# Performance work log

Hardware: AMD Instinct MI355X
Metric: run time of the kernel (lower is better)

The kernel has to match this reference:

```python
import jax, jax.numpy as jnp
from jax import lax
import numpy as np

B, P, T = 2048, 128, 64     # batch, program len, trace len
V, NC, NO = 1000, 32, 16    # token vocab, n choice names, options per choice
E, H = 300, 256             # embedding size, hidden size
GIN = H + 2 * E             # GRUCell input size = 856


def setup_inputs() -> dict:
    key = jax.random.key(0)
    ks = jax.random.split(key, 20)
    g = lambda k, shape, fan: jax.random.normal(k, shape, jnp.float32) / np.sqrt(fan)
    return {
        "program": jax.random.randint(ks[0], (B, P), 0, V),
        "program_len": jax.random.randint(ks[1], (B,), 1, P + 1),
        "trace": jax.random.randint(ks[2], (B, T), 0, NC),
        "trace_len": jax.random.randint(ks[3], (B,), 1, T + 1),
        "choices": jax.random.randint(ks[4], (B, NC), 0, NO),
        "h0_enc": jax.random.normal(ks[5], (B, H), jnp.float32) * 0.06,  # xavier-ish init of h0
        "h0_dec": jax.random.normal(ks[6], (B, H), jnp.float32) * 0.06,
        "token_emb": jax.random.normal(ks[7], (V, E), jnp.float32) * 0.02,
        "Wih_enc": g(ks[8], (H, E), E),      # vanilla RNN (tanh)
        "Whh_enc": g(ks[9], (H, H), H),
        "bih_enc": jnp.zeros((H,), jnp.float32),
        "bhh_enc": jnp.zeros((H,), jnp.float32),
        "choice_tab": jax.random.normal(ks[10], (NC, NO, E), jnp.float32) * 0.02,
        "index_tab": jax.random.normal(ks[11], (NC, E), jnp.float32) * 0.02,
        "Wih_gru": g(ks[12], (3 * H, GIN), GIN),
        "Whh_gru": g(ks[13], (3 * H, H), H),
        "bih_gru": jnp.zeros((3 * H,), jnp.float32),
        "bhh_gru": jnp.zeros((3 * H,), jnp.float32),
        "infW": g(ks[14], (NC, NO, H), H),   # per-choice-name Linear(H -> NO)
        "infb": jnp.zeros((NC, NO), jnp.float32),
    }


def _encode(program, program_len, h0, token_emb, Wih, Whh, bih, bhh):
    # ProgramEncoder: embedding -> packed tanh-RNN -> final hidden per sequence
    xs = jnp.swapaxes(token_emb[program], 0, 1)            # [P, B, E] time-major
    mask = jnp.arange(P)[:, None] < program_len[None, :]   # [P, B] valid steps

    def step(h, inp):
        x_t, m_t = inp
        h_new = jnp.tanh(x_t @ Wih.T + bih + h @ Whh.T + bhh)
        return jnp.where(m_t[:, None], h_new, h), None

    h_final, _ = lax.scan(step, h0, (xs, mask))
    return h_final  # [B, H]


def reference(program, program_len, trace, trace_len, choices, h0_enc, h0_dec,
              token_emb, Wih_enc, Whh_enc, bih_enc, bhh_enc,
              choice_tab, index_tab, Wih_gru, Whh_gru, bih_gru, bhh_gru,
              infW, infb):
    prog_h = _encode(program, program_len, h0_enc, token_emb,
                     Wih_enc, Whh_enc, bih_enc, bhh_enc)      # [B, H]

    prev_seq = jnp.swapaxes(trace[:, :-1], 0, 1)  # [T-1, B] choice-name at step i
    cur_seq = jnp.swapaxes(trace[:, 1:], 0, 1)    # [T-1, B] choice-name at step i+1
    barange = jnp.arange(B)

    def dec_step(h, inp):
        prev, cur = inp                           # [B] ints
        idx_e = index_tab[prev]                   # [B, E]
        opt = choices[barange, prev]              # gather(dim=1) of chosen option
        ch_e = choice_tab[prev, opt]              # [B, E]
        x = jnp.concatenate([ch_e, prog_h, idx_e], axis=-1)  # [B, GIN]
        # GRUCell (torch gate order r, z, n)
        gx = x @ Wih_gru.T + bih_gru              # [B, 3H]
        gh = h @ Whh_gru.T + bhh_gru
        xr, xz, xn = jnp.split(gx, 3, axis=-1)
        hr, hz, hn = jnp.split(gh, 3, axis=-1)
        r = jax.nn.sigmoid(xr + hr)
        z = jax.nn.sigmoid(xz + hz)
        n = jnp.tanh(xn + r * hn)
        h_new = (1.0 - z) * n + z * h
        # per-choice-name inference head selected by cur_choice
        pred = jnp.einsum('bh,boh->bo', h_new, infW[cur]) + infb[cur]  # [B, NO]
        return h_new, pred

    _, preds = lax.scan(dec_step, h0_dec, (prev_seq, cur_seq))
    return preds  # [T-1, B, NO]
```

## Files before the change

kernel.cpp:

```cpp
#include <hip/hip_runtime.h>


typedef unsigned short ushort_t;
typedef short short8 __attribute__((ext_vector_type(8)));
typedef float f32x4_t __attribute__((ext_vector_type(4)));

#define NB_ 128

__device__ __forceinline__ ushort_t f32_to_bf16_rne(float f){
    unsigned int u = __float_as_uint(f);
    unsigned int r = u + 0x7fffu + ((u >> 16) & 1u);
    return (ushort_t)(r >> 16);
}
__device__ __forceinline__ float b2f(ushort_t s){
    return __uint_as_float(((unsigned int)s) << 16);
}
__device__ __forceinline__ void split2(float x, ushort_t &hh, ushort_t &hl){
    hh = f32_to_bf16_rne(x);
    float r = x - b2f(hh);
    hl = f32_to_bf16_rne(r);
}
__device__ __forceinline__ f32x4_t mfma16(uint4 a, uint4 b, f32x4_t c){
    return __builtin_amdgcn_mfma_f32_16x16x32_bf16(
        __builtin_bit_cast(short8, a), __builtin_bit_cast(short8, b), c, 0, 0, 0);
}
__device__ __forceinline__ float sigm(float x){
    return __fdividef(1.f, 1.f + __expf(-x));
}
__device__ __forceinline__ float tanh_f(float x){
    return 1.f - __fdividef(2.f, 1.f + __expf(2.f * x));
}

__global__ void prep_kernel(
    const float* __restrict__ Whh_enc, const float* __restrict__ Whh_gru,
    const float* __restrict__ Wih_gru, const float* __restrict__ token_emb,
    const float* __restrict__ Wih_enc, const float* __restrict__ bih_enc,
    const float* __restrict__ bhh_enc, const float* __restrict__ index_tab,
    const float* __restrict__ bih_gru, const float* __restrict__ bhh_gru,
    const float* __restrict__ choice_tab,
    ushort_t* __restrict__ enc_h, ushort_t* __restrict__ enc_l,
    ushort_t* __restrict__ gru_h, ushort_t* __restrict__ gru_l,
    ushort_t* __restrict__ mid_h, ushort_t* __restrict__ mid_l,
    float* __restrict__ tok_proj, float* __restrict__ xproj)
{
    __shared__ __align__(16) float s_a[304];
    __shared__ __align__(16) float s_b[304];
    const int tid = threadIdx.x;
    const int bid = blockIdx.x;

    if (bid < 1792){
        const int idx = bid * 256 + tid;
        float v; ushort_t *ph, *pl; int fi;
        if (idx < 65536){
            fi = idx;
            const int m = fi & 7, lane = (fi >> 3) & 63, t2 = fi >> 9;
            const int nt = t2 & 15, kt = t2 >> 4;
            const int k = (kt << 5) + ((lane >> 4) << 3) + m;
            const int j = (nt << 4) + (lane & 15);
            v = Whh_enc[(j << 8) + k]; ph = enc_h; pl = enc_l;
        } else if (idx < 262144){
            fi = idx - 65536;
            const int m = fi & 7, lane = (fi >> 3) & 63, t2 = fi >> 9;
            const int nt = t2 % 48, kt = t2 / 48;
            const int k = (kt << 5) + ((lane >> 4) << 3) + m;
            const int j = (nt << 4) + (lane & 15);
            v = Whh_gru[(j << 8) + k]; ph = gru_h; pl = gru_l;
        } else {
            fi = idx - 262144;
            const int m = fi & 7, lane = (fi >> 3) & 63, t2 = fi >> 9;
            const int nt = t2 % 48, kt = t2 / 48;
            const int k = (kt << 5) + ((lane >> 4) << 3) + m;
            const int j = (nt << 4) + (lane & 15);
            v = Wih_gru[j * 856 + 300 + k]; ph = mid_h; pl = mid_l;
        }
        ushort_t hh, hl; split2(v, hh, hl);
        ph[fi] = hh; pl[fi] = hl;
    } else if (bid < 3328){
        const int b2 = bid - 1792;
        const int co = b2 / 3, part = b2 - co * 3;
        const int c = co >> 4;
        const int g = part * 256 + tid;
        for (int i2 = tid; i2 < 300; i2 += 256){
            s_a[i2] = choice_tab[co * 300 + i2];
            s_b[i2] = index_tab[c * 300 + i2];
        }
        __syncthreads();
        float acc = bih_gru[g] + (g < 512 ? bhh_gru[g] : 0.f);
        const f32x4_t* wa = (const f32x4_t*)(Wih_gru + g * 856);
        const f32x4_t* wb = (const f32x4_t*)(Wih_gru + g * 856 + 556);
        const f32x4_t* xa = (const f32x4_t*)s_a;
        const f32x4_t* xb = (const f32x4_t*)s_b;
        #pragma unroll 5
        for (int e = 0; e < 75; ++e){
            f32x4_t a = xa[e], w0 = wa[e], b = xb[e], w1 = wb[e];
            acc += a[0]*w0[0] + a[1]*w0[1] + a[2]*w0[2] + a[3]*w0[3]
                 + b[0]*w1[0] + b[1]*w1[1] + b[2]*w1[2] + b[3]*w1[3];
        }
        xproj[co * 768 + g] = acc;
    } else {
        const int v0 = bid - 3328;
        for (int i2 = tid; i2 < 300; i2 += 256) s_a[i2] = token_emb[v0 * 300 + i2];
        __syncthreads();
        float acc = bih_enc[tid] + bhh_enc[tid];
        const f32x4_t* wa = (const f32x4_t*)(Wih_enc + tid * 300);
        const f32x4_t* xa = (const f32x4_t*)s_a;
        #pragma unroll 5
        for (int e = 0; e < 75; ++e){
            f32x4_t a = xa[e], b = wa[e];
            acc += a[0]*b[0] + a[1]*b[1] + a[2]*b[2] + a[3]*b[3];
        }
        tok_proj[(v0 << 8) + tid] = acc;
    }
}

__global__ __launch_bounds__(256, 1) void enc_kernel(
    const int* __restrict__ program, const int* __restrict__ plen,
    const float* __restrict__ h0, const float* __restrict__ tokproj,
    const ushort_t* __restrict__ enc_h, const ushort_t* __restrict__ enc_l,
    const ushort_t* __restrict__ mid_h, const ushort_t* __restrict__ mid_l,
    float* __restrict__ prog_proj)
{
    __shared__ __align__(16) ushort_t hbuf[2][2][16 * 256];
    __shared__ int prog_s[16 * 128];
    const int tid = threadIdx.x, bid = blockIdx.x;
    const int wave = tid >> 6, lane = tid & 63;
    const int r0 = bid << 4;

    for (int i = tid; i < 2048; i += 256) prog_s[i] = program[(r0 << 7) + i];

    const int rowbase = (lane >> 4) << 2;
    const int jbase = (wave << 6) + (lane & 15);
    int plen_r[4];
    #pragma unroll
    for (int i = 0; i < 4; ++i) plen_r[i] = plen[r0 + rowbase + i];

    const uint4* __restrict__ be_h = (const uint4*)enc_h;
    const uint4* __restrict__ be_l = (const uint4*)enc_l;
    uint4 bh_r[8][4], bl_r[8][4];
    #pragma unroll
    for (int kt = 0; kt < 8; ++kt)
    #pragma unroll
    for (int q = 0; q < 4; ++q){
        const int fo = (((kt << 4) + (wave << 2) + q) << 6) + lane;
        bh_r[kt][q] = be_h[fo];
        bl_r[kt][q] = be_l[fo];
    }

    float hreg[4][4];
    #pragma unroll
    for (int q = 0; q < 4; ++q)
    #pragma unroll
    for (int i = 0; i < 4; ++i){
        const int row = rowbase + i, j = jbase + (q << 4);
        float v = h0[((r0 + row) << 8) + j];
        hreg[q][i] = v;
        ushort_t hh, hl; split2(v, hh, hl);
        const int b0 = (((row << 9) + (j << 1)) ^ ((row & 7) << 4)) >> 1;
        hbuf[0][0][b0] = hh; hbuf[0][1][b0] = hl;
    }
    __syncthreads();

    const int arow = lane & 15;
    const int abase = (arow << 9) + ((lane >> 4) << 4);
    const int asw = (arow & 7) << 4;
    int cur = 0;

    for (int t = 0; t < 128; ++t){
        f32x4_t acc[4];
        int tok[4];
        #pragma unroll
        for (int i = 0; i < 4; ++i) tok[i] = prog_s[((rowbase + i) << 7) + t];
        #pragma unroll
        for (int q = 0; q < 4; ++q)
        #pragma unroll
        for (int i = 0; i < 4; ++i)
            acc[q][i] = tokproj[(tok[i] << 8) + jbase + (q << 4)];

        #pragma unroll
        for (int kt = 0; kt < 8; ++kt){
            const int b = ((abase + (kt << 6)) ^ asw) >> 1;
            const uint4 ah = *(const uint4*)&hbuf[cur][0][b];
            const uint4 al = *(const uint4*)&hbuf[cur][1][b];
            #pragma unroll
            for (int q = 0; q < 4; ++q){
                f32x4_t c = acc[q];
                c = mfma16(ah, bh_r[kt][q], c);
                c = mfma16(al, bh_r[kt][q], c);
                c = mfma16(ah, bl_r[kt][q], c);
                acc[q] = c;
            }
        }
        const int nb = cur ^ 1;
        #pragma unroll
        for (int q = 0; q < 4; ++q)
        #pragma unroll
        for (int i = 0; i < 4; ++i){
            const int row = rowbase + i, j = jbase + (q << 4);
            float v = (t < plen_r[i]) ? tanh_f(acc[q][i]) : hreg[q][i];
            hreg[q][i] = v;
            ushort_t hh, hl; split2(v, hh, hl);
            const int b0 = (((row << 9) + (j << 1)) ^ ((row & 7) << 4)) >> 1;
            hbuf[nb][0][b0] = hh; hbuf[nb][1][b0] = hl;
        }
        cur = nb;
        __syncthreads();
    }

    uint4 ahr[8], alr[8];
    #pragma unroll
    for (int kt = 0; kt < 8; ++kt){
        const int b = ((abase + (kt << 6)) ^ asw) >> 1;
        ahr[kt] = *(const uint4*)&hbuf[cur][0][b];
        alr[kt] = *(const uint4*)&hbuf[cur][1][b];
    }
    const uint4* __restrict__ bm_h = (const uint4*)mid_h;
    const uint4* __restrict__ bm_l = (const uint4*)mid_l;
    f32x4_t pacc[12];
    #pragma unroll
    for (int u = 0; u < 12; ++u){ f32x4_t z = {0.f,0.f,0.f,0.f}; pacc[u] = z; }
    #pragma unroll
    for (int kt = 0; kt < 8; ++kt){
        #pragma unroll
        for (int u = 0; u < 12; ++u){
            const int nt = wave * 12 + u;
            const int fo = ((kt * 48 + nt) << 6) + lane;
            const uint4 bh = bm_h[fo], bl = bm_l[fo];
            f32x4_t c = pacc[u];
            c = mfma16(ahr[kt], bh, c);
            c = mfma16(alr[kt], bh, c);
            c = mfma16(ahr[kt], bl, c);
            pacc[u] = c;
        }
    }
    #pragma unroll
    for (int u = 0; u < 12; ++u){
        const int g = (wave * 12 + u) * 16 + (lane & 15);
        #pragma unroll
        for (int i = 0; i < 4; ++i)
            prog_proj[(r0 + rowbase + i) * 768 + g] = pacc[u][i];
    }
}

__global__ __launch_bounds__(256, 1) void dec_kernel(
    const int* __restrict__ trace, const int* __restrict__ choices,
    const float* __restrict__ h0, const float* __restrict__ prog_proj,
    const float* __restrict__ xproj,
    const ushort_t* __restrict__ gru_h, const ushort_t* __restrict__ gru_l,
    const float* __restrict__ bhh_gru, const float* __restrict__ infW,
    const float* __restrict__ infb, float* __restrict__ out)
{
    __shared__ __align__(16) ushort_t hbuf[2][2][16 * 256];
    __shared__ __align__(16) float pred_lds[16 * 272];
    __shared__ int trace_s[16 * 64];
    __shared__ int choice_s[16 * 32];
    const int tid = threadIdx.x, bid = blockIdx.x;
    const int wave = tid >> 6, lane = tid & 63;
    const int r0 = bid << 4;

    for (int i = tid; i < 1024; i += 256) trace_s[i] = trace[(r0 << 6) + i];
    for (int i = tid; i < 512; i += 256) choice_s[i] = choices[(r0 << 5) + i];

    const int rowbase = (lane >> 4) << 2;
    const int jbase = (wave << 6) + (lane & 15);

    float hreg[4][4];
    float bhhn[4];
    #pragma unroll
    for (int q = 0; q < 4; ++q) bhhn[q] = bhh_gru[512 + jbase + (q << 4)];

    float ppr[3][4][4];
    #pragma unroll
    for (int g3 = 0; g3 < 3; ++g3)
    #pragma unroll
    for (int q = 0; q < 4; ++q)
    #pragma unroll
    for (int i = 0; i < 4; ++i)
        ppr[g3][q][i] = prog_proj[(r0 + rowbase + i) * 768 + (g3 << 8) + jbase + (q << 4)];

    #pragma unroll
    for (int q = 0; q < 4; ++q)
    #pragma unroll
    for (int i = 0; i < 4; ++i){
        const int row = rowbase + i, j = jbase + (q << 4);
        float v = h0[((r0 + row) << 8) + j];
        hreg[q][i] = v;
        ushort_t hh, hl; split2(v, hh, hl);
        const int b0 = (((row << 9) + (j << 1)) ^ ((row & 7) << 4)) >> 1;
        hbuf[0][0][b0] = hh; hbuf[0][1][b0] = hl;
    }
    __syncthreads();

    const uint4* __restrict__ bg_h = (const uint4*)gru_h;
    const uint4* __restrict__ bg_l = (const uint4*)gru_l;
    const int arow = lane & 15;
    const int abase = (arow << 9) + ((lane >> 4) << 4);
    const int asw = (arow & 7) << 4;
    int cur = 0;

    for (int t = 0; t < 63; ++t){
        int prev_i[4], opt_i[4];
        #pragma unroll
        for (int i = 0; i < 4; ++i){
            const int row = rowbase + i;
            prev_i[i] = trace_s[(row << 6) + t];
            opt_i[i] = choice_s[(row << 5) + prev_i[i]];
        }
        f32x4_t acc[3][4];
        float xn[4][4];
        #pragma unroll
        for (int i = 0; i < 4; ++i){
            const float* xp = xproj + ((prev_i[i] << 4) + opt_i[i]) * 768;
            #pragma unroll
            for (int q = 0; q < 4; ++q){
                const int j = jbase + (q << 4);
                acc[0][q][i] = xp[j]       + ppr[0][q][i];
                acc[1][q][i] = xp[256 + j] + ppr[1][q][i];
                xn[q][i]     = xp[512 + j] + ppr[2][q][i];
                acc[2][q][i] = bhhn[q];
            }
        }
        uint4 ahr[8], alr[8];
        #pragma unroll
        for (int kt = 0; kt < 8; ++kt){
            const int b = ((abase + (kt << 6)) ^ asw) >> 1;
            ahr[kt] = *(const uint4*)&hbuf[cur][0][b];
            alr[kt] = *(const uint4*)&hbuf[cur][1][b];
        }
        #pragma unroll
        for (int kt = 0; kt < 8; ++kt){
            #pragma unroll
            for (int g3 = 0; g3 < 3; ++g3)
            #pragma unroll
            for (int q = 0; q < 4; ++q){
                const int nt = (g3 << 4) + (wave << 2) + q;
                const int fo = ((kt * 48 + nt) << 6) + lane;
                const uint4 bh = bg_h[fo], bl = bg_l[fo];
                f32x4_t c = acc[g3][q];
                c = mfma16(ahr[kt], bh, c);
                c = mfma16(alr[kt], bh, c);
                c = mfma16(ahr[kt], bl, c);
                acc[g3][q] = c;
            }
        }
        const int nb = cur ^ 1;
        #pragma unroll
        for (int q = 0; q < 4; ++q)
        #pragma unroll
        for (int i = 0; i < 4; ++i){
            const float r = sigm(acc[0][q][i]);
            const float z = sigm(acc[1][q][i]);
            const float n = tanh_f(xn[q][i] + r * acc[2][q][i]);
            const float hv = (1.f - z) * n + z * hreg[q][i];
            hreg[q][i] = hv;
            ushort_t hh, hl; split2(hv, hh, hl);
            const int row = rowbase + i, j = jbase + (q << 4);
            const int b0 = (((row << 9) + (j << 1)) ^ ((row & 7) << 4)) >> 1;
            hbuf[nb][0][b0] = hh; hbuf[nb][1][b0] = hl;
        }
        __syncthreads();

        {
            const int prow = tid >> 4, ks = tid & 15;
            const int ct = trace_s[(prow << 6) + t + 1];
            const int psw = (prow & 7) << 4;
            const int hb = (prow << 9) + (ks << 5);
            union { uint4 v; ushort_t s[8]; } H0, H1, L0, L1;
            H0.v = *(const uint4*)&hbuf[nb][0][((hb) ^ psw) >> 1];
            H1.v = *(const uint4*)&hbuf[nb][0][((hb + 16) ^ psw) >> 1];
            L0.v = *(const uint4*)&hbuf[nb][1][((hb) ^ psw) >> 1];
            L1.v = *(const uint4*)&hbuf[nb][1][((hb + 16) ^ psw) >> 1];
            float hv[16];
            #pragma unroll
            for (int n2 = 0; n2 < 8; ++n2){
                hv[n2]     = b2f(H0.s[n2]) + b2f(L0.s[n2]);
                hv[8 + n2] = b2f(H1.s[n2]) + b2f(L1.s[n2]);
            }
            const float* iwb = infW + ((size_t)ct << 12) + (ks << 4);
            #pragma unroll
            for (int o = 0; o < 16; ++o){
                const f32x4_t* wp = (const f32x4_t*)(iwb + (o << 8));
                const f32x4_t w0 = wp[0], w1 = wp[1], w2 = wp[2], w3 = wp[3];
                float s =
                    hv[0]*w0[0] + hv[1]*w0[1] + hv[2]*w0[2] + hv[3]*w0[3]
                  + hv[4]*w1[0] + hv[5]*w1[1] + hv[6]*w1[2] + hv[7]*w1[3]
                  + hv[8]*w2[0] + hv[9]*w2[1] + hv[10]*w2[2] + hv[11]*w2[3]
                  + hv[12]*w3[0]+ hv[13]*w3[1]+ hv[14]*w3[2]+ hv[15]*w3[3];
                pred_lds[prow * 272 + (o << 4) + ks] = s;
            }
        }
        __syncthreads();
        {
            const int rrow = tid >> 4, oo = tid & 15;
            float s = 0.f;
            #pragma unroll
            for (int k2 = 0; k2 < 16; ++k2) s += pred_lds[rrow * 272 + (oo << 4) + k2];
            const int ct2 = trace_s[(rrow << 6) + t + 1];
            s += infb[(ct2 << 4) + oo];
            out[(size_t)t * 32768 + ((size_t)(r0 + rrow) << 4) + oo] = s;
        }
        cur = nb;
    }
}

extern "C" void kernel_launch(void* const* d_in, const int* in_sizes, int n_in,
                              void* d_out, int out_size, void* d_ws, size_t ws_size,
                              hipStream_t stream)
{
    const int*   program   = (const int*)  d_in[0];
    const int*   plen      = (const int*)  d_in[1];
    const int*   trace     = (const int*)  d_in[2];
    const int*   choices   = (const int*)  d_in[4];
    const float* h0_enc    = (const float*)d_in[5];
    const float* h0_dec    = (const float*)d_in[6];
    const float* token_emb = (const float*)d_in[7];
    const float* Wih_enc   = (const float*)d_in[8];
    const float* Whh_enc   = (const float*)d_in[9];
    const float* bih_enc   = (const float*)d_in[10];
    const float* bhh_enc   = (const float*)d_in[11];
    const float* choice_tab= (const float*)d_in[12];
    const float* index_tab = (const float*)d_in[13];
    const float* Wih_gru   = (const float*)d_in[14];
    const float* Whh_gru   = (const float*)d_in[15];
    const float* bih_gru   = (const float*)d_in[16];
    const float* bhh_gru   = (const float*)d_in[17];
    const float* infW      = (const float*)d_in[18];
    const float* infb      = (const float*)d_in[19];
    float* out = (float*)d_out;

    char* w = (char*)d_ws;
    ushort_t* enc_h = (ushort_t*)(w + 0);
    ushort_t* enc_l = (ushort_t*)(w + 131072);
    ushort_t* gru_h = (ushort_t*)(w + 262144);
    ushort_t* gru_l = (ushort_t*)(w + 655360);
    ushort_t* mid_h = (ushort_t*)(w + 1048576);
    ushort_t* mid_l = (ushort_t*)(w + 1441792);
    float* tok_proj = (float*)(w + 1835008);
    float* xproj    = (float*)(w + 2859008);
    float* prog_proj= (float*)(w + 4431872);

    prep_kernel<<<4328, 256, 0, stream>>>(
        Whh_enc, Whh_gru, Wih_gru, token_emb, Wih_enc, bih_enc, bhh_enc,
        index_tab, bih_gru, bhh_gru, choice_tab,
        enc_h, enc_l, gru_h, gru_l, mid_h, mid_l,
        tok_proj, xproj);

    enc_kernel<<<NB_, 256, 0, stream>>>(
        program, plen, h0_enc, tok_proj, enc_h, enc_l, mid_h, mid_l, prog_proj);

    dec_kernel<<<NB_, 256, 0, stream>>>(
        trace, choices, h0_dec, prog_proj, xproj,
        gru_h, gru_l, bhh_gru, infW, infb, out);
}
```

Before: 3.648 ms.

## Retile GRU decoder to 32 rows per block and prefetch encoder token projections

```diff
diff --git a/kernel.cpp b/kernel.cpp
--- a/kernel.cpp
+++ b/kernel.cpp
@@ -4,8 +4,6 @@
 typedef unsigned short ushort_t;
 typedef short short8 __attribute__((ext_vector_type(8)));
 typedef float f32x4_t __attribute__((ext_vector_type(4)));
-
-#define NB_ 128
 
 __device__ __forceinline__ ushort_t f32_to_bf16_rne(float f){
     unsigned int u = __float_as_uint(f);
@@ -165,16 +163,36 @@
     const int asw = (arow & 7) << 4;
     int cur = 0;
 
+    float nxt[4][4];
+    {
+        int tok[4];
+        #pragma unroll
+        for (int i = 0; i < 4; ++i) tok[i] = prog_s[((rowbase + i) << 7)];
+        #pragma unroll
+        for (int q = 0; q < 4; ++q)
+        #pragma unroll
+        for (int i = 0; i < 4; ++i)
+            nxt[q][i] = tokproj[(tok[i] << 8) + jbase + (q << 4)];
+    }
+
     for (int t = 0; t < 128; ++t){
         f32x4_t acc[4];
-        int tok[4];
-        #pragma unroll
-        for (int i = 0; i < 4; ++i) tok[i] = prog_s[((rowbase + i) << 7) + t];
         #pragma unroll
         for (int q = 0; q < 4; ++q)
         #pragma unroll
         for (int i = 0; i < 4; ++i)
-            acc[q][i] = tokproj[(tok[i] << 8) + jbase + (q << 4)];
+            acc[q][i] = nxt[q][i];
+
+        if (t < 127){
+            int tok[4];
+            #pragma unroll
+            for (int i = 0; i < 4; ++i) tok[i] = prog_s[((rowbase + i) << 7) + t + 1];
+            #pragma unroll
+            for (int q = 0; q < 4; ++q)
+            #pragma unroll
+            for (int i = 0; i < 4; ++i)
+                nxt[q][i] = tokproj[(tok[i] << 8) + jbase + (q << 4)];
+        }
 
         #pragma unroll
         for (int kt = 0; kt < 8; ++kt){
@@ -241,7 +259,7 @@
     }
 }
 
-__global__ __launch_bounds__(256, 1) void dec_kernel(
+__global__ __launch_bounds__(512, 2) void dec_kernel(
     const int* __restrict__ trace, const int* __restrict__ choices,
     const float* __restrict__ h0, const float* __restrict__ prog_proj,
     const float* __restrict__ xproj,
@@ -249,45 +267,39 @@
     const float* __restrict__ bhh_gru, const float* __restrict__ infW,
     const float* __restrict__ infb, float* __restrict__ out)
 {
-    __shared__ __align__(16) ushort_t hbuf[2][2][16 * 256];
-    __shared__ __align__(16) float pred_lds[16 * 272];
-    __shared__ int trace_s[16 * 64];
-    __shared__ int choice_s[16 * 32];
+    __shared__ __align__(16) ushort_t hbuf[2][32 * 256];
+    __shared__ int trace_s[32 * 64];
+    __shared__ int choice_s[32 * 32];
     const int tid = threadIdx.x, bid = blockIdx.x;
     const int wave = tid >> 6, lane = tid & 63;
-    const int r0 = bid << 4;
-
-    for (int i = tid; i < 1024; i += 256) trace_s[i] = trace[(r0 << 6) + i];
-    for (int i = tid; i < 512; i += 256) choice_s[i] = choices[(r0 << 5) + i];
-
-    const int rowbase = (lane >> 4) << 2;
-    const int jbase = (wave << 6) + (lane & 15);
-
-    float hreg[4][4];
-    float bhhn[4];
-    #pragma unroll
-    for (int q = 0; q < 4; ++q) bhhn[q] = bhh_gru[512 + jbase + (q << 4)];
-
-    float ppr[3][4][4];
-    #pragma unroll
-    for (int g3 = 0; g3 < 3; ++g3)
-    #pragma unroll
-    for (int q = 0; q < 4; ++q)
-    #pragma unroll
-    for (int i = 0; i < 4; ++i)
-        ppr[g3][q][i] = prog_proj[(r0 + rowbase + i) * 768 + (g3 << 8) + jbase + (q << 4)];
-
-    #pragma unroll
-    for (int q = 0; q < 4; ++q)
-    #pragma unroll
-    for (int i = 0; i < 4; ++i){
-        const int row = rowbase + i, j = jbase + (q << 4);
+    const int r0 = bid << 5;
+
+    for (int i = tid; i < 2048; i += 512) trace_s[i] = trace[(r0 << 6) + i];
+    for (int i = tid; i < 1024; i += 512) choice_s[i] = choices[(r0 << 5) + i];
+
+    #pragma unroll
+    for (int e = 0; e < 16; ++e){
+        const int i = (e << 9) + tid;
+        const int row = i >> 8, j = i & 255;
         float v = h0[((r0 + row) << 8) + j];
-        hreg[q][i] = v;
         ushort_t hh, hl; split2(v, hh, hl);
         const int b0 = (((row << 9) + (j << 1)) ^ ((row & 7) << 4)) >> 1;
-        hbuf[0][0][b0] = hh; hbuf[0][1][b0] = hl;
-    }
+        hbuf[0][b0] = hh; hbuf[1][b0] = hl;
+    }
+
+    const int crow = (lane >> 4) << 2;
+    const int jcol = (wave << 5) + (lane & 15);
+    float bhhn[2];
+    #pragma unroll
+    for (int jt = 0; jt < 2; ++jt) bhhn[jt] = bhh_gru[512 + jcol + (jt << 4)];
+    float hreg[2][2][4];
+    #pragma unroll
+    for (int rt = 0; rt < 2; ++rt)
+    #pragma unroll
+    for (int jt = 0; jt < 2; ++jt)
+    #pragma unroll
+    for (int rg = 0; rg < 4; ++rg)
+        hreg[rt][jt][rg] = h0[((r0 + (rt << 4) + crow + rg) << 8) + jcol + (jt << 4)];
     __syncthreads();
 
     const uint4* __restrict__ bg_h = (const uint4*)gru_h;
@@ -295,67 +307,96 @@
     const int arow = lane & 15;
     const int abase = (arow << 9) + ((lane >> 4) << 4);
     const int asw = (arow & 7) << 4;
-    int cur = 0;
 
     for (int t = 0; t < 63; ++t){
-        int prev_i[4], opt_i[4];
-        #pragma unroll
-        for (int i = 0; i < 4; ++i){
-            const int row = rowbase + i;
-            prev_i[i] = trace_s[(row << 6) + t];
-            opt_i[i] = choice_s[(row << 5) + prev_i[i]];
-        }
-        f32x4_t acc[3][4];
-        float xn[4][4];
-        #pragma unroll
-        for (int i = 0; i < 4; ++i){
-            const float* xp = xproj + ((prev_i[i] << 4) + opt_i[i]) * 768;
-            #pragma unroll
-            for (int q = 0; q < 4; ++q){
-                const int j = jbase + (q << 4);
-                acc[0][q][i] = xp[j]       + ppr[0][q][i];
-                acc[1][q][i] = xp[256 + j] + ppr[1][q][i];
-                xn[q][i]     = xp[512 + j] + ppr[2][q][i];
-                acc[2][q][i] = bhhn[q];
-            }
-        }
-        uint4 ahr[8], alr[8];
-        #pragma unroll
-        for (int kt = 0; kt < 8; ++kt){
-            const int b = ((abase + (kt << 6)) ^ asw) >> 1;
-            ahr[kt] = *(const uint4*)&hbuf[cur][0][b];
-            alr[kt] = *(const uint4*)&hbuf[cur][1][b];
-        }
-        #pragma unroll
-        for (int kt = 0; kt < 8; ++kt){
-            #pragma unroll
-            for (int g3 = 0; g3 < 3; ++g3)
-            #pragma unroll
-            for (int q = 0; q < 4; ++q){
-                const int nt = (g3 << 4) + (wave << 2) + q;
-                const int fo = ((kt * 48 + nt) << 6) + lane;
-                const uint4 bh = bg_h[fo], bl = bg_l[fo];
-                f32x4_t c = acc[g3][q];
-                c = mfma16(ahr[kt], bh, c);
-                c = mfma16(alr[kt], bh, c);
-                c = mfma16(ahr[kt], bl, c);
-                acc[g3][q] = c;
-            }
-        }
-        const int nb = cur ^ 1;
-        #pragma unroll
-        for (int q = 0; q < 4; ++q)
-        #pragma unroll
-        for (int i = 0; i < 4; ++i){
-            const float r = sigm(acc[0][q][i]);
-            const float z = sigm(acc[1][q][i]);
-            const float n = tanh_f(xn[q][i] + r * acc[2][q][i]);
-            const float hv = (1.f - z) * n + z * hreg[q][i];
-            hreg[q][i] = hv;
-            ushort_t hh, hl; split2(hv, hh, hl);
-            const int row = rowbase + i, j = jbase + (q << 4);
+        f32x4_t acc[3][2][2];
+        #pragma unroll
+        for (int rt = 0; rt < 2; ++rt)
+        #pragma unroll
+        for (int jt = 0; jt < 2; ++jt){
+            f32x4_t z4 = {0.f, 0.f, 0.f, 0.f};
+            acc[0][rt][jt] = z4; acc[1][rt][jt] = z4;
+            f32x4_t bn = {bhhn[jt], bhhn[jt], bhhn[jt], bhhn[jt]};
+            acc[2][rt][jt] = bn;
+        }
+
+        float xv[3][2][2][4];
+        #pragma unroll
+        for (int half = 0; half < 2; ++half){
+            if (half == 1){
+                #pragma unroll
+                for (int rt = 0; rt < 2; ++rt)
+                #pragma unroll
+                for (int rg = 0; rg < 4; ++rg){
+                    const int lrow = (rt << 4) + crow + rg;
+                    const int prev = trace_s[(lrow << 6) + t];
+                    const int opt = choice_s[(lrow << 5) + prev];
+                    const float* xb = xproj + ((prev << 4) + opt) * 768;
+                    const float* pb = prog_proj + (r0 + lrow) * 768;
+                    #pragma unroll
+                    for (int g = 0; g < 3; ++g)
+                    #pragma unroll
+                    for (int jt = 0; jt < 2; ++jt){
+                        const int jj = (g << 8) + jcol + (jt << 4);
+                        xv[g][rt][jt][rg] = xb[jj] + pb[jj];
+                    }
+                }
+            }
+            #pragma unroll
+            for (int kt4 = 0; kt4 < 4; ++kt4){
+                const int kt = (half << 2) + kt4;
+                uint4 ah[2], al[2];
+                #pragma unroll
+                for (int rt = 0; rt < 2; ++rt){
+                    const int b = (((rt << 13) + abase + (kt << 6)) ^ asw) >> 1;
+                    ah[rt] = *(const uint4*)&hbuf[0][b];
+                    al[rt] = *(const uint4*)&hbuf[1][b];
+                }
+                #pragma unroll
+                for (int g = 0; g < 3; ++g)
+                #pragma unroll
+                for (int jt = 0; jt < 2; ++jt){
+                    const int nt = (g << 4) + (wave << 1) + jt;
+                    const int fo = ((kt * 48 + nt) << 6) + lane;
+                    const uint4 bh = bg_h[fo], bl = bg_l[fo];
+                    #pragma unroll
+                    for (int rt = 0; rt < 2; ++rt){
+                        f32x4_t c = acc[g][rt][jt];
+                        c = mfma16(ah[rt], bh, c);
+                        c = mfma16(al[rt], bh, c);
+                        c = mfma16(ah[rt], bl, c);
+                        acc[g][rt][jt] = c;
+                    }
+                }
+            }
+        }
+
+        ushort_t wh[2][2][4], wl[2][2][4];
+        #pragma unroll
+        for (int rt = 0; rt < 2; ++rt)
+        #pragma unroll
+        for (int jt = 0; jt < 2; ++jt)
+        #pragma unroll
+        for (int rg = 0; rg < 4; ++rg){
+            const float rr = sigm(acc[0][rt][jt][rg] + xv[0][rt][jt][rg]);
+            const float zz = sigm(acc[1][rt][jt][rg] + xv[1][rt][jt][rg]);
+            const float nn = tanh_f(xv[2][rt][jt][rg] + rr * acc[2][rt][jt][rg]);
+            const float hv = (1.f - zz) * nn + zz * hreg[rt][jt][rg];
+            hreg[rt][jt][rg] = hv;
+            split2(hv, wh[rt][jt][rg], wl[rt][jt][rg]);
+        }
+        __syncthreads();
+        #pragma unroll
+        for (int rt = 0; rt < 2; ++rt)
+        #pragma unroll
+        for (int jt = 0; jt < 2; ++jt)
+        #pragma unroll
+        for (int rg = 0; rg < 4; ++rg){
+            const int row = (rt << 4) + crow + rg;
+            const int j = jcol + (jt << 4);
             const int b0 = (((row << 9) + (j << 1)) ^ ((row & 7) << 4)) >> 1;
-            hbuf[nb][0][b0] = hh; hbuf[nb][1][b0] = hl;
+            hbuf[0][b0] = wh[rt][jt][rg];
+            hbuf[1][b0] = wl[rt][jt][rg];
         }
         __syncthreads();
 
@@ -363,42 +404,45 @@
             const int prow = tid >> 4, ks = tid & 15;
             const int ct = trace_s[(prow << 6) + t + 1];
             const int psw = (prow & 7) << 4;
-            const int hb = (prow << 9) + (ks << 5);
-            union { uint4 v; ushort_t s[8]; } H0, H1, L0, L1;
-            H0.v = *(const uint4*)&hbuf[nb][0][((hb) ^ psw) >> 1];
-            H1.v = *(const uint4*)&hbuf[nb][0][((hb + 16) ^ psw) >> 1];
-            L0.v = *(const uint4*)&hbuf[nb][1][((hb) ^ psw) >> 1];
-            L1.v = *(const uint4*)&hbuf[nb][1][((hb + 16) ^ psw) >> 1];
-            float hv[16];
+            const int ba = (((prow << 9) + (ks << 5)) ^ psw) >> 1;
+            const int bb = (((prow << 9) + (ks << 5) + 16) ^ psw) >> 1;
+            union { uint4 v; ushort_t u[8]; } H0, H1, L0, L1;
+            H0.v = *(const uint4*)&hbuf[0][ba];
+            H1.v = *(const uint4*)&hbuf[0][bb];
+            L0.v = *(const uint4*)&hbuf[1][ba];
+            L1.v = *(const uint4*)&hbuf[1][bb];
+            float hv16[16];
             #pragma unroll
             for (int n2 = 0; n2 < 8; ++n2){
-                hv[n2]     = b2f(H0.s[n2]) + b2f(L0.s[n2]);
-                hv[8 + n2] = b2f(H1.s[n2]) + b2f(L1.s[n2]);
+                hv16[n2]     = b2f(H0.u[n2]) + b2f(L0.u[n2]);
+                hv16[8 + n2] = b2f(H1.u[n2]) + b2f(L1.u[n2]);
             }
             const float* iwb = infW + ((size_t)ct << 12) + (ks << 4);
+            float s[16];
             #pragma unroll
             for (int o = 0; o < 16; ++o){
                 const f32x4_t* wp = (const f32x4_t*)(iwb + (o << 8));
                 const f32x4_t w0 = wp[0], w1 = wp[1], w2 = wp[2], w3 = wp[3];
-                float s =
-                    hv[0]*w0[0] + hv[1]*w0[1] + hv[2]*w0[2] + hv[3]*w0[3]
-                  + hv[4]*w1[0] + hv[5]*w1[1] + hv[6]*w1[2] + hv[7]*w1[3]
-                  + hv[8]*w2[0] + hv[9]*w2[1] + hv[10]*w2[2] + hv[11]*w2[3]
-                  + hv[12]*w3[0]+ hv[13]*w3[1]+ hv[14]*w3[2]+ hv[15]*w3[3];
-                pred_lds[prow * 272 + (o << 4) + ks] = s;
-            }
-        }
-        __syncthreads();
-        {
-            const int rrow = tid >> 4, oo = tid & 15;
-            float s = 0.f;
-            #pragma unroll
-            for (int k2 = 0; k2 < 16; ++k2) s += pred_lds[rrow * 272 + (oo << 4) + k2];
-            const int ct2 = trace_s[(rrow << 6) + t + 1];
-            s += infb[(ct2 << 4) + oo];
-            out[(size_t)t * 32768 + ((size_t)(r0 + rrow) << 4) + oo] = s;
-        }
-        cur = nb;
+                s[o] =
+                    hv16[0]*w0[0] + hv16[1]*w0[1] + hv16[2]*w0[2] + hv16[3]*w0[3]
+                  + hv16[4]*w1[0] + hv16[5]*w1[1] + hv16[6]*w1[2] + hv16[7]*w1[3]
+                  + hv16[8]*w2[0] + hv16[9]*w2[1] + hv16[10]*w2[2]+ hv16[11]*w2[3]
+                  + hv16[12]*w3[0]+ hv16[13]*w3[1]+ hv16[14]*w3[2]+ hv16[15]*w3[3];
+            }
+            #pragma unroll
+            for (int m = 1; m < 16; m <<= 1){
+                const int keep_hi = ks & m;
+                #pragma unroll
+                for (int i = 0; i < 16 / (m * 2); ++i){
+                    const float a = s[2*i], b = s[2*i + 1];
+                    const float axx = __shfl_xor(a, m);
+                    const float bxx = __shfl_xor(b, m);
+                    s[i] = keep_hi ? (b + bxx) : (a + axx);
+                }
+            }
+            out[(size_t)t * 32768 + ((size_t)(r0 + prow) << 4) + ks] =
+                s[0] + infb[(ct << 4) + ks];
+        }
     }
 }
 
@@ -444,10 +488,10 @@
         enc_h, enc_l, gru_h, gru_l, mid_h, mid_l,
         tok_proj, xproj);
 
-    enc_kernel<<<NB_, 256, 0, stream>>>(
+    enc_kernel<<<128, 256, 0, stream>>>(
         program, plen, h0_enc, tok_proj, enc_h, enc_l, mid_h, mid_l, prog_proj);
 
-    dec_kernel<<<NB_, 256, 0, stream>>>(
+    dec_kernel<<<64, 512, 0, stream>>>(
         trace, choices, h0_dec, prog_proj, xproj,
         gru_h, gru_l, bhh_gru, infW, infb, out);
 }
```

New measurement: 3.455 ms. 5.3% less time.
